# Kernel optimization log

Measured on AMD Instinct MI355X. Metric: run time of the kernel, lower is better.

## Reference

```python
import jax, jax.numpy as jnp
import numpy as np

D_MODEL = 1024
N_HEADS = 16
D_K = D_MODEL // N_HEADS
CAUSAL = True


def setup_inputs() -> dict:
    key = jax.random.key(0)
    ks = jax.random.split(key, 11)
    B, S, D = 2, 2048, D_MODEL
    scale = 1.0 / np.sqrt(D)
    inp = {
        "in_Q": jax.random.normal(ks[0], (B, S, D), jnp.float32),
        "in_K": jax.random.normal(ks[1], (B, S, D), jnp.float32),
        "in_V": jax.random.normal(ks[2], (B, S, D), jnp.float32),
        # torch Linear params: weight [out, in], bias [out]
        "Wq": jax.random.normal(ks[3], (D, D), jnp.float32) * scale,
        "bq": jax.random.normal(ks[4], (D,), jnp.float32) * scale,
        "Wk": jax.random.normal(ks[5], (D, D), jnp.float32) * scale,
        "bk": jax.random.normal(ks[6], (D,), jnp.float32) * scale,
        "Wv": jax.random.normal(ks[7], (D, D), jnp.float32) * scale,
        "bv": jax.random.normal(ks[8], (D,), jnp.float32) * scale,
        "Wo": jax.random.normal(ks[9], (D, D), jnp.float32) * scale,
        "bo": jax.random.normal(ks[10], (D,), jnp.float32) * scale,
    }
    return inp


def reference(in_Q, in_K, in_V, Wq, bq, Wk, bk, Wv, bv, Wo, bo):
    B, S, D = in_Q.shape
    H, dk = N_HEADS, D_K
    # Linear projections (torch: x @ W.T + b)
    Q = in_Q @ Wq.T + bq
    K = in_K @ Wk.T + bk
    V = in_V @ Wv.T + bv
    # split heads: [B, S, D] -> [B, H, S, dk]
    Qh = Q.reshape(B, S, H, dk).transpose(0, 2, 1, 3)
    Kh = K.reshape(B, S, H, dk).transpose(0, 2, 1, 3)
    Vh = V.reshape(B, S, H, dk).transpose(0, 2, 1, 3)
    # scores [B, H, S, S]
    scores = jnp.einsum("bhqd,bhkd->bhqk", Qh, Kh) / jnp.sqrt(jnp.float32(dk))
    if CAUSAL:
        mask = jnp.tril(jnp.ones((S, S), dtype=bool))
        scores = jnp.where(mask, scores, -jnp.inf)
    attn = jax.nn.softmax(scores, axis=-1)
    out = jnp.einsum("bhqk,bhkd->bhqd", attn, Vh)
    Hcat = out.transpose(0, 2, 1, 3).reshape(B, S, D)
    return Hcat @ Wo.T + bo
```

## Files before the change

### kernel.cpp

```cpp
#include <hip/hip_runtime.h>
#include <hip/hip_bf16.h>
#include <math.h>

#define D_MODEL 1024
#define NHEADS  16
#define DK      64
#define SEQ     2048
#define BATCH   2
#define MROWS   4096
#define NQT     (SEQ/64)

typedef unsigned short ushort_t;
using short8 = __attribute__((ext_vector_type(8))) short;
using f32x4  = __attribute__((ext_vector_type(4))) float;

__device__ __forceinline__ ushort_t f2bf(float x) {
    unsigned u = __float_as_uint(x);
    u = (u + 0x7FFFu + ((u >> 16) & 1u)) >> 16;
    return (ushort_t)u;
}

__device__ __forceinline__ unsigned pk2(float a, float b) {
    __hip_bfloat162 h = __float22bfloat162_rn(float2{a, b});
    unsigned u;
    __builtin_memcpy(&u, &h, 4);
    return u;
}

__device__ __forceinline__ void gll16(const ushort_t* g, ushort_t* l) {
    __builtin_amdgcn_global_load_lds(
        (const __attribute__((address_space(1))) void*)(g),
        (__attribute__((address_space(3))) void*)(l), 16, 0, 0);
}

__global__ __launch_bounds__(256) void cvt_bf16(
    const float* s0, const float* s1, const float* s2, const float* s3,
    const float* s4, const float* s5, const float* s6,
    ushort_t* d0, ushort_t* d1, ushort_t* d2, ushort_t* d3,
    ushort_t* d4, ushort_t* d5, ushort_t* d6, int nIn, int nW)
{
    const float* s; ushort_t* d; int n;
    switch (blockIdx.y) {
        case 0: s = s0; d = d0; n = nIn; break;
        case 1: s = s1; d = d1; n = nIn; break;
        case 2: s = s2; d = d2; n = nIn; break;
        case 3: s = s3; d = d3; n = nW;  break;
        case 4: s = s4; d = d4; n = nW;  break;
        case 5: s = s5; d = d5; n = nW;  break;
        default: s = s6; d = d6; n = nW; break;
    }
    int i = (blockIdx.x * 256 + threadIdx.x) * 4;
    if (i < n) {
        float4 v = *(const float4*)&s[i];
        ushort4 o;
        o.x = f2bf(v.x); o.y = f2bf(v.y); o.z = f2bf(v.z); o.w = f2bf(v.w);
        *(ushort4*)&d[i] = o;
    }
}

struct GemmArgs { const ushort_t* A; const ushort_t* W; const float* bias;
                  void* C; int mode; float oscale; };

template<int MODE>
__device__ __forceinline__ void gemm_core(const GemmArgs& ga,
                                          ushort_t* As, ushort_t* Bs)
{
    constexpr bool SWP = (MODE != 1);
    const int tid  = threadIdx.x;
    const int w    = tid >> 6, lane = tid & 63;
    const int quad = lane >> 4, lx = lane & 15;
    const int mw = (w >> 1) * 64, nw = (w & 1) * 64;
    const int bm = blockIdx.x * 128, bn = blockIdx.y * 128;
    const int K = D_MODEL;

    f32x4 acc[4][4];
#pragma unroll
    for (int mt = 0; mt < 4; ++mt)
#pragma unroll
        for (int nt = 0; nt < 4; ++nt)
            acc[mt][nt] = (f32x4){0.f, 0.f, 0.f, 0.f};

    float4 b4[4];
    float  bfr[4];
#pragma unroll
    for (int nt = 0; nt < 4; ++nt) {
        if (SWP) b4[nt] = *(const float4*)&ga.bias[bn + nw + nt * 16 + quad * 4];
        else     bfr[nt] = ga.bias[bn + nw + nt * 16 + lx];
    }

    for (int k0 = 0; k0 < K; k0 += 64) {
        __syncthreads();
#pragma unroll
        for (int i = 0; i < 4; ++i) {
            int r0 = (w * 4 + i) * 8;
            int rl = r0 + (lane >> 3);
            int g  = (lane & 7) ^ (rl & 7);
            gll16(&ga.A[(size_t)(bm + rl) * K + k0 + g * 8], &As[r0 * 64]);
            gll16(&ga.W[(size_t)(bn + rl) * K + k0 + g * 8], &Bs[r0 * 64]);
        }
        __syncthreads();

#pragma unroll
        for (int ks = 0; ks < 2; ++ks) {
            short8 af[4], bf[4];
#pragma unroll
            for (int mt = 0; mt < 4; ++mt) {
                int r = mw + mt * 16 + lx;
                af[mt] = *(const short8*)&As[r * 64 + (((ks * 4 + quad) ^ (r & 7)) << 3)];
            }
#pragma unroll
            for (int nt = 0; nt < 4; ++nt) {
                int r = nw + nt * 16 + lx;
                bf[nt] = *(const short8*)&Bs[r * 64 + (((ks * 4 + quad) ^ (r & 7)) << 3)];
            }
#pragma unroll
            for (int mt = 0; mt < 4; ++mt)
#pragma unroll
                for (int nt = 0; nt < 4; ++nt)
                    acc[mt][nt] = SWP
                        ? __builtin_amdgcn_mfma_f32_16x16x32_bf16(bf[nt], af[mt], acc[mt][nt], 0, 0, 0)
                        : __builtin_amdgcn_mfma_f32_16x16x32_bf16(af[mt], bf[nt], acc[mt][nt], 0, 0, 0);
        }
    }

    if (MODE == 0) {
        ushort_t* C = (ushort_t*)ga.C;
        const float os = ga.oscale;
#pragma unroll
        for (int mt = 0; mt < 4; ++mt) {
            int m = bm + mw + mt * 16 + lx;
#pragma unroll
            for (int nt = 0; nt < 4; ++nt) {
                int n0 = bn + nw + nt * 16 + quad * 4;
                uint2 u;
                u.x = pk2((acc[mt][nt][0] + b4[nt].x) * os, (acc[mt][nt][1] + b4[nt].y) * os);
                u.y = pk2((acc[mt][nt][2] + b4[nt].z) * os, (acc[mt][nt][3] + b4[nt].w) * os);
                *(uint2*)&C[(size_t)m * D_MODEL + n0] = u;
            }
        }
    } else if (MODE == 2) {
        float* C = (float*)ga.C;
#pragma unroll
        for (int mt = 0; mt < 4; ++mt) {
            int m = bm + mw + mt * 16 + lx;
#pragma unroll
            for (int nt = 0; nt < 4; ++nt) {
                int n0 = bn + nw + nt * 16 + quad * 4;
                float4 v;
                v.x = acc[mt][nt][0] + b4[nt].x;
                v.y = acc[mt][nt][1] + b4[nt].y;
                v.z = acc[mt][nt][2] + b4[nt].z;
                v.w = acc[mt][nt][3] + b4[nt].w;
                *(float4*)&C[(size_t)m * D_MODEL + n0] = v;
            }
        }
    } else {
        ushort_t* C = (ushort_t*)ga.C;
#pragma unroll
        for (int mt = 0; mt < 4; ++mt)
#pragma unroll
            for (int nt = 0; nt < 4; ++nt) {
                int n = bn + nw + nt * 16 + lx;
                int d = n & 63, h = n >> 6;
                int m0 = bm + mw + mt * 16 + quad * 4;
                int b = m0 >> 11, s0 = m0 & 2047;
                uint2 u;
                u.x = pk2(acc[mt][nt][0] + bfr[nt], acc[mt][nt][1] + bfr[nt]);
                u.y = pk2(acc[mt][nt][2] + bfr[nt], acc[mt][nt][3] + bfr[nt]);
                *(uint2*)&C[((size_t)(b * NHEADS + h) * DK + d) * SEQ + s0] = u;
            }
    }
}

__global__ __launch_bounds__(256) void gemm_mfma(GemmArgs g0, GemmArgs g1, GemmArgs g2)
{
    __shared__ ushort_t As[128 * 64];
    __shared__ ushort_t Bs[128 * 64];
    GemmArgs ga = (blockIdx.z == 0) ? g0 : ((blockIdx.z == 1) ? g1 : g2);
    if (ga.mode == 0)      gemm_core<0>(ga, As, Bs);
    else if (ga.mode == 1) gemm_core<1>(ga, As, Bs);
    else                   gemm_core<2>(ga, As, Bs);
}

__device__ __forceinline__ void flash_tile(
    int qt, const size_t qbase, const size_t vbase,
    const ushort_t* __restrict__ Qp, const ushort_t* __restrict__ Kp,
    const ushort_t* __restrict__ Vt, ushort_t* __restrict__ Hc,
    ushort_t* Ks0, ushort_t* Ks1, ushort_t* Vs0, ushort_t* Vs1,
    ushort_t (*Ps)[16 * 72])
{
    const int tid  = threadIdx.x;
    const int w    = tid >> 6, lane = tid & 63;
    const int quad = lane >> 4, lx = lane & 15;

    asm volatile("s_barrier" ::: "memory");

    {
#pragma unroll
        for (int i = 0; i < 2; ++i) {
            int r0 = (w + i * 4) * 8;
            int rl = r0 + (lane >> 3);
            int g  = (lane & 7) ^ (rl & 7);
            gll16(&Kp[qbase + (size_t)(0 * 64 + rl) * D_MODEL + g * 8], &Ks0[r0 * 64]);
            gll16(&Vt[vbase + (size_t)rl * SEQ + 0 * 64 + g * 8], &Vs0[r0 * 64]);
        }
    }

    short8 qf[2];
    {
        size_t ro = qbase + (size_t)(qt * 64 + w * 16 + lx) * D_MODEL + quad * 8;
        qf[0] = *(const short8*)&Qp[ro];
        qf[1] = *(const short8*)&Qp[ro + 32];
    }

    f32x4 O[4];
#pragma unroll
    for (int nt = 0; nt < 4; ++nt) O[nt] = (f32x4){0.f, 0.f, 0.f, 0.f};
    float mrow = -INFINITY, lrow = 0.f;
    const int qin = w * 16 + lx;

    for (int kt = 0; kt <= qt; ++kt) {
        ushort_t* Ks = (kt & 1) ? Ks1 : Ks0;
        ushort_t* Vs = (kt & 1) ? Vs1 : Vs0;

        asm volatile("s_waitcnt vmcnt(0)" ::: "memory");
        asm volatile("s_barrier" ::: "memory");

        if (kt < qt) {
            ushort_t* Kn = (kt & 1) ? Ks0 : Ks1;
            ushort_t* Vn = (kt & 1) ? Vs0 : Vs1;
#pragma unroll
            for (int i = 0; i < 2; ++i) {
                int r0 = (w + i * 4) * 8;
                int rl = r0 + (lane >> 3);
                int g  = (lane & 7) ^ (rl & 7);
                gll16(&Kp[qbase + (size_t)((kt + 1) * 64 + rl) * D_MODEL + g * 8], &Kn[r0 * 64]);
                gll16(&Vt[vbase + (size_t)rl * SEQ + (kt + 1) * 64 + g * 8], &Vn[r0 * 64]);
            }
        }

        f32x4 s[4];
#pragma unroll
        for (int nt = 0; nt < 4; ++nt) {
            int r = nt * 16 + lx;
            short8 kf0 = *(const short8*)&Ks[r * 64 + ((quad ^ (r & 7)) << 3)];
            short8 kf1 = *(const short8*)&Ks[r * 64 + (((4 + quad) ^ (r & 7)) << 3)];
            f32x4 z = (f32x4){0.f, 0.f, 0.f, 0.f};
            z = __builtin_amdgcn_mfma_f32_16x16x32_bf16(kf0, qf[0], z, 0, 0, 0);
            z = __builtin_amdgcn_mfma_f32_16x16x32_bf16(kf1, qf[1], z, 0, 0, 0);
            s[nt] = z;
        }

        if (kt == qt) {
#pragma unroll
            for (int nt = 0; nt < 4; ++nt)
#pragma unroll
                for (int r = 0; r < 4; ++r)
                    if ((nt * 16 + quad * 4 + r) > qin) s[nt][r] = -INFINITY;
        }

        float tm = -INFINITY;
#pragma unroll
        for (int nt = 0; nt < 4; ++nt)
#pragma unroll
            for (int r = 0; r < 4; ++r) tm = fmaxf(tm, s[nt][r]);
        tm = fmaxf(tm, __shfl_xor(tm, 16, 64));
        tm = fmaxf(tm, __shfl_xor(tm, 32, 64));
        float mnew = fmaxf(mrow, tm);
        float alpha = __builtin_amdgcn_exp2f(mrow - mnew);
        mrow = mnew;
        float rs = 0.f;
#pragma unroll
        for (int nt = 0; nt < 4; ++nt)
#pragma unroll
            for (int r = 0; r < 4; ++r) {
                float p = __builtin_amdgcn_exp2f(s[nt][r] - mnew);
                s[nt][r] = p;
                rs += p;
            }
        rs += __shfl_xor(rs, 16, 64);
        rs += __shfl_xor(rs, 32, 64);
        lrow = lrow * alpha + rs;
#pragma unroll
        for (int nt = 0; nt < 4; ++nt)
#pragma unroll
            for (int r = 0; r < 4; ++r) O[nt][r] *= alpha;

#pragma unroll
        for (int nt = 0; nt < 4; ++nt) {
            uint2 u;
            u.x = pk2(s[nt][0], s[nt][1]);
            u.y = pk2(s[nt][2], s[nt][3]);
            *(uint2*)&Ps[w][lx * 72 + nt * 16 + quad * 4] = u;
        }

        short8 pf0 = *(const short8*)&Ps[w][lx * 72 + quad * 8];
        short8 pf1 = *(const short8*)&Ps[w][lx * 72 + 32 + quad * 8];

#pragma unroll
        for (int nt = 0; nt < 4; ++nt) {
            int r = nt * 16 + lx;
            short8 vf0 = *(const short8*)&Vs[r * 64 + ((quad ^ (r & 7)) << 3)];
            short8 vf1 = *(const short8*)&Vs[r * 64 + (((4 + quad) ^ (r & 7)) << 3)];
            O[nt] = __builtin_amdgcn_mfma_f32_16x16x32_bf16(vf0, pf0, O[nt], 0, 0, 0);
            O[nt] = __builtin_amdgcn_mfma_f32_16x16x32_bf16(vf1, pf1, O[nt], 0, 0, 0);
        }
    }

    {
        float invl = 1.f / lrow;
        size_t ro = qbase + (size_t)(qt * 64 + w * 16 + lx) * D_MODEL;
#pragma unroll
        for (int nt = 0; nt < 4; ++nt) {
            uint2 u;
            u.x = pk2(O[nt][0] * invl, O[nt][1] * invl);
            u.y = pk2(O[nt][2] * invl, O[nt][3] * invl);
            *(uint2*)&Hc[ro + nt * 16 + quad * 4] = u;
        }
    }
}

__global__ __launch_bounds__(256) void flash_mfma(
    const ushort_t* __restrict__ Qp, const ushort_t* __restrict__ Kp,
    const ushort_t* __restrict__ Vt, ushort_t* __restrict__ Hc)
{
    const int p  = blockIdx.x;
    const int bh = blockIdx.y;
    const int b = bh >> 4, h = bh & 15;

    __shared__ ushort_t Ks0[64 * 64], Ks1[64 * 64];
    __shared__ ushort_t Vs0[64 * 64], Vs1[64 * 64];
    __shared__ ushort_t Ps[4][16 * 72];

    const size_t qbase = (size_t)(b * SEQ) * D_MODEL + h * DK;
    const size_t vbase = (size_t)bh * DK * SEQ;

    flash_tile(NQT - 1 - p, qbase, vbase, Qp, Kp, Vt, Hc, Ks0, Ks1, Vs0, Vs1, Ps);
    flash_tile(p,           qbase, vbase, Qp, Kp, Vt, Hc, Ks0, Ks1, Vs0, Vs1, Ps);
}

extern "C" void kernel_launch(void* const* d_in, const int* in_sizes, int n_in,
                              void* d_out, int out_size, void* d_ws, size_t ws_size,
                              hipStream_t stream) {
    const float* inQ = (const float*)d_in[0];
    const float* inK = (const float*)d_in[1];
    const float* inV = (const float*)d_in[2];
    const float* Wq  = (const float*)d_in[3];
    const float* bq  = (const float*)d_in[4];
    const float* Wk  = (const float*)d_in[5];
    const float* bk  = (const float*)d_in[6];
    const float* Wv  = (const float*)d_in[7];
    const float* bv  = (const float*)d_in[8];
    const float* Wo  = (const float*)d_in[9];
    const float* bo  = (const float*)d_in[10];
    float* out = (float*)d_out;

    const size_t NI = (size_t)MROWS * D_MODEL;
    const size_t NW = (size_t)D_MODEL * D_MODEL;
    ushort_t* ws  = (ushort_t*)d_ws;
    ushort_t* Qb  = ws;
    ushort_t* Kb  = Qb  + NI;
    ushort_t* Vb  = Kb  + NI;
    ushort_t* Wqb = Vb  + NI;
    ushort_t* Wkb = Wqb + NW;
    ushort_t* Wvb = Wkb + NW;
    ushort_t* Wob = Wvb + NW;
    ushort_t* Qp  = Wob + NW;
    ushort_t* Kp  = Qp  + NI;
    ushort_t* Vtg = Kp  + NI;
    ushort_t* Hc  = Vtg + NI;

    cvt_bf16<<<dim3(NI / 1024, 7), 256, 0, stream>>>(
        inQ, inK, inV, Wq, Wk, Wv, Wo,
        Qb, Kb, Vb, Wqb, Wkb, Wvb, Wob, (int)NI, (int)NW);

    const float qsc = 0.125f * 1.44269504088896340736f;
    GemmArgs aq{Qb, Wqb, bq, (void*)Qp, 0, qsc};
    GemmArgs ak{Kb, Wkb, bk, (void*)Kp, 0, 1.0f};
    GemmArgs av{Vb, Wvb, bv, (void*)Vtg, 1, 1.0f};
    gemm_mfma<<<dim3(MROWS / 128, D_MODEL / 128, 3), 256, 0, stream>>>(aq, ak, av);

    flash_mfma<<<dim3(NQT / 2, BATCH * NHEADS), 256, 0, stream>>>(Qp, Kp, Vtg, Hc);

    GemmArgs ao{Hc, Wob, bo, (void*)out, 2, 1.0f};
    gemm_mfma<<<dim3(MROWS / 128, D_MODEL / 128, 1), 256, 0, stream>>>(ao, ao, ao);
}
```

Baseline: 226.1 us.

## Double-buffer GEMM LDS tiles and remap flash blocks across XCDs

The projection GEMM now uses two LDS buffers for its A and W tiles and prefetches the next K tile while the MFMAs run on the current one. This hides global-load latency behind compute at the cost of twice the LDS per block, which may lower occupancy. The flash attention grid is flattened to one dimension and remapped so that blocks sharing a batch-head land on the same XCD, which should improve L2 reuse of K and V.

```diff
diff --git a/kernel.cpp b/kernel.cpp
--- a/kernel.cpp
+++ b/kernel.cpp
@@ -63,7 +63,8 @@
 
 template<int MODE>
 __device__ __forceinline__ void gemm_core(const GemmArgs& ga,
-                                          ushort_t* As, ushort_t* Bs)
+                                          ushort_t* As0, ushort_t* Bs0,
+                                          ushort_t* As1, ushort_t* Bs1)
 {
     constexpr bool SWP = (MODE != 1);
     const int tid  = threadIdx.x;
@@ -73,23 +74,7 @@
     const int bm = blockIdx.x * 128, bn = blockIdx.y * 128;
     const int K = D_MODEL;
 
-    f32x4 acc[4][4];
-#pragma unroll
-    for (int mt = 0; mt < 4; ++mt)
-#pragma unroll
-        for (int nt = 0; nt < 4; ++nt)
-            acc[mt][nt] = (f32x4){0.f, 0.f, 0.f, 0.f};
-
-    float4 b4[4];
-    float  bfr[4];
-#pragma unroll
-    for (int nt = 0; nt < 4; ++nt) {
-        if (SWP) b4[nt] = *(const float4*)&ga.bias[bn + nw + nt * 16 + quad * 4];
-        else     bfr[nt] = ga.bias[bn + nw + nt * 16 + lx];
-    }
-
-    for (int k0 = 0; k0 < K; k0 += 64) {
-        __syncthreads();
+    auto stage = [&](int k0, ushort_t* As, ushort_t* Bs) {
 #pragma unroll
         for (int i = 0; i < 4; ++i) {
             int r0 = (w * 4 + i) * 8;
@@ -98,7 +83,34 @@
             gll16(&ga.A[(size_t)(bm + rl) * K + k0 + g * 8], &As[r0 * 64]);
             gll16(&ga.W[(size_t)(bn + rl) * K + k0 + g * 8], &Bs[r0 * 64]);
         }
-        __syncthreads();
+    };
+
+    f32x4 acc[4][4];
+#pragma unroll
+    for (int mt = 0; mt < 4; ++mt)
+#pragma unroll
+        for (int nt = 0; nt < 4; ++nt)
+            acc[mt][nt] = (f32x4){0.f, 0.f, 0.f, 0.f};
+
+    float4 b4[4];
+    float  bfr[4];
+#pragma unroll
+    for (int nt = 0; nt < 4; ++nt) {
+        if (SWP) b4[nt] = *(const float4*)&ga.bias[bn + nw + nt * 16 + quad * 4];
+        else     bfr[nt] = ga.bias[bn + nw + nt * 16 + lx];
+    }
+
+    stage(0, As0, Bs0);
+
+    for (int it = 0; it < K / 64; ++it) {
+        ushort_t* As = (it & 1) ? As1 : As0;
+        ushort_t* Bs = (it & 1) ? Bs1 : Bs0;
+
+        asm volatile("s_waitcnt vmcnt(0)" ::: "memory");
+        asm volatile("s_barrier" ::: "memory");
+
+        if (it + 1 < K / 64)
+            stage((it + 1) * 64, (it & 1) ? As0 : As1, (it & 1) ? Bs0 : Bs1);
 
 #pragma unroll
         for (int ks = 0; ks < 2; ++ks) {
@@ -174,12 +186,12 @@
 
 __global__ __launch_bounds__(256) void gemm_mfma(GemmArgs g0, GemmArgs g1, GemmArgs g2)
 {
-    __shared__ ushort_t As[128 * 64];
-    __shared__ ushort_t Bs[128 * 64];
+    __shared__ ushort_t As0[128 * 64], Bs0[128 * 64];
+    __shared__ ushort_t As1[128 * 64], Bs1[128 * 64];
     GemmArgs ga = (blockIdx.z == 0) ? g0 : ((blockIdx.z == 1) ? g1 : g2);
-    if (ga.mode == 0)      gemm_core<0>(ga, As, Bs);
-    else if (ga.mode == 1) gemm_core<1>(ga, As, Bs);
-    else                   gemm_core<2>(ga, As, Bs);
+    if (ga.mode == 0)      gemm_core<0>(ga, As0, Bs0, As1, Bs1);
+    else if (ga.mode == 1) gemm_core<1>(ga, As0, Bs0, As1, Bs1);
+    else                   gemm_core<2>(ga, As0, Bs0, As1, Bs1);
 }
 
 __device__ __forceinline__ void flash_tile(
@@ -201,8 +213,8 @@
             int r0 = (w + i * 4) * 8;
             int rl = r0 + (lane >> 3);
             int g  = (lane & 7) ^ (rl & 7);
-            gll16(&Kp[qbase + (size_t)(0 * 64 + rl) * D_MODEL + g * 8], &Ks0[r0 * 64]);
-            gll16(&Vt[vbase + (size_t)rl * SEQ + 0 * 64 + g * 8], &Vs0[r0 * 64]);
+            gll16(&Kp[qbase + (size_t)rl * D_MODEL + g * 8], &Ks0[r0 * 64]);
+            gll16(&Vt[vbase + (size_t)rl * SEQ + g * 8], &Vs0[r0 * 64]);
         }
     }
 
@@ -324,8 +336,11 @@
     const ushort_t* __restrict__ Qp, const ushort_t* __restrict__ Kp,
     const ushort_t* __restrict__ Vt, ushort_t* __restrict__ Hc)
 {
-    const int p  = blockIdx.x;
-    const int bh = blockIdx.y;
+    const int id  = blockIdx.x;
+    const int xcd = id & 7;
+    const int k   = id >> 3;
+    const int bh  = (xcd << 2) | (k & 3);
+    const int p   = k >> 2;
     const int b = bh >> 4, h = bh & 15;
 
     __shared__ ushort_t Ks0[64 * 64], Ks1[64 * 64];
@@ -380,7 +395,7 @@
     GemmArgs av{Vb, Wvb, bv, (void*)Vtg, 1, 1.0f};
     gemm_mfma<<<dim3(MROWS / 128, D_MODEL / 128, 3), 256, 0, stream>>>(aq, ak, av);
 
-    flash_mfma<<<dim3(NQT / 2, BATCH * NHEADS), 256, 0, stream>>>(Qp, Kp, Vtg, Hc);
+    flash_mfma<<<dim3(NQT / 2 * BATCH * NHEADS), 256, 0, stream>>>(Qp, Kp, Vtg, Hc);
 
     GemmArgs ao{Hc, Wob, bo, (void*)out, 2, 1.0f};
     gemm_mfma<<<dim3(MROWS / 128, D_MODEL / 128, 1), 256, 0, stream>>>(ao, ao, ao);
```

Result: no change. 228.5 us (+1.1%).
